# Kernel optimization log

Hardware: AMD Instinct MI355X
Metric: run time of the kernel (lower is better)

Reference implementation:

```python
import jax, jax.numpy as jnp
import numpy as np

STATE_DIM = 256
LATENT_DIM = 64
HIDDEN = 64
NUM_EMB = 2048
BATCH = 32768


def setup_inputs() -> dict:
    key = jax.random.key(0)
    ks = jax.random.split(key, 10)
    s = lambda *sh: 1.0 / np.sqrt(sh[0])
    return {
        "x": jax.random.normal(ks[0], (BATCH, STATE_DIM), dtype=jnp.float32),
        # encoder: Linear(state_dim, 64) -> ReLU -> Linear(64, latent_dim)
        "enc_w1": jax.random.uniform(ks[1], (STATE_DIM, HIDDEN), jnp.float32, -s(STATE_DIM), s(STATE_DIM)),
        "enc_b1": jax.random.uniform(ks[2], (HIDDEN,), jnp.float32, -s(STATE_DIM), s(STATE_DIM)),
        "enc_w2": jax.random.uniform(ks[3], (HIDDEN, LATENT_DIM), jnp.float32, -s(HIDDEN), s(HIDDEN)),
        "enc_b2": jax.random.uniform(ks[4], (LATENT_DIM,), jnp.float32, -s(HIDDEN), s(HIDDEN)),
        # codebook
        "emb": jax.random.normal(ks[5], (NUM_EMB, LATENT_DIM), dtype=jnp.float32),
        # decoder: Linear(latent_dim, 64) -> ReLU -> Linear(64, state_dim)
        "dec_w1": jax.random.uniform(ks[6], (LATENT_DIM, HIDDEN), jnp.float32, -s(LATENT_DIM), s(LATENT_DIM)),
        "dec_b1": jax.random.uniform(ks[7], (HIDDEN,), jnp.float32, -s(LATENT_DIM), s(LATENT_DIM)),
        "dec_w2": jax.random.uniform(ks[8], (HIDDEN, STATE_DIM), jnp.float32, -s(HIDDEN), s(HIDDEN)),
        "dec_b2": jax.random.uniform(ks[9], (STATE_DIM,), jnp.float32, -s(HIDDEN), s(HIDDEN)),
    }


def reference(x, enc_w1, enc_b1, enc_w2, enc_b2, emb, dec_w1, dec_b1, dec_w2, dec_b2):
    # encoder MLP: z_e [B, latent]
    h = jax.nn.relu(x @ enc_w1 + enc_b1)
    z_e = h @ enc_w2 + enc_b2
    # squared euclidean distances to codebook, expanded form: [B, K]
    # ||z - e||^2 = ||z||^2 - 2 z.e + ||e||^2  (same argmin as broadcast form)
    d = (jnp.sum(z_e * z_e, axis=1, keepdims=True)
         - 2.0 * (z_e @ emb.T)
         + jnp.sum(emb * emb, axis=1)[None, :])
    z_q_idx = jnp.argmin(d, axis=1)           # [B]
    z_q = emb[z_q_idx]                        # [B, latent]
    # decoder MLP
    hd = jax.nn.relu(z_q @ dec_w1 + dec_b1)
    x_recon = hd @ dec_w2 + dec_b2
    return (x_recon, z_e, z_q)
```

## Files before the change

### kernel.cpp

```cpp
#include <hip/hip_runtime.h>

#define BATCH   32768
#define SD      256
#define LD      64
#define HDIM    64
#define NEMB    2048
#define REFINE_THR_Q 5e-4f

typedef short  short8 __attribute__((ext_vector_type(8)));
typedef float  f32x4  __attribute__((ext_vector_type(4)));

__device__ __forceinline__ unsigned short f2bf(float f) {
    unsigned int u = __float_as_uint(f);
    u = (u + 0x7FFFu + ((u >> 16) & 1u)) >> 16;
    return (unsigned short)u;
}
__device__ __forceinline__ float bf2f(unsigned short h) {
    return __uint_as_float(((unsigned int)h) << 16);
}

__global__ __launch_bounds__(256) void k0_all(const float* __restrict__ emb,
                                              const float* __restrict__ dw1,
                                              const float* __restrict__ dw2,
                                              const float* __restrict__ ew1,
                                              const float* __restrict__ ew2,
                                              float* __restrict__ e2q,
                                              unsigned short* __restrict__ eh,
                                              unsigned short* __restrict__ el,
                                              unsigned short* __restrict__ w1h,
                                              unsigned short* __restrict__ w1l,
                                              unsigned short* __restrict__ w2h,
                                              unsigned short* __restrict__ w2l,
                                              unsigned short* __restrict__ w1eh,
                                              unsigned short* __restrict__ w1em,
                                              unsigned short* __restrict__ w1el,
                                              unsigned short* __restrict__ w2eh,
                                              unsigned short* __restrict__ w2em,
                                              unsigned short* __restrict__ w2el,
                                              int* __restrict__ count) {
    int b = blockIdx.x;
    int t = threadIdx.x;
    if (b < 8) {
        int k = b * 256 + t;
        if (k == 0) *count = 0;
        const float* er = emb + (size_t)k * LD;
        unsigned short hrow[LD], lrow[LD];
        float s = 0.f;
#pragma unroll
        for (int q = 0; q < LD; ++q) {
            float v = er[q];
            s += v * v;
            unsigned short h = f2bf(v);
            hrow[q] = h;
            lrow[q] = f2bf(v - bf2f(h));
        }
        e2q[k] = -0.5f * s;
        short8* dh = (short8*)(eh + (size_t)k * LD);
        short8* dl = (short8*)(el + (size_t)k * LD);
#pragma unroll
        for (int q = 0; q < 8; ++q) {
            dh[q] = *(short8*)&hrow[q * 8];
            dl[q] = *(short8*)&lrow[q * 8];
        }
    } else if (b < 24) {
        int e = (b - 8) * 256 + t;
        int j = e >> 6, k = e & 63;
        float v = dw1[k * HDIM + j];
        unsigned short h = f2bf(v);
        w1h[e] = h; w1l[e] = f2bf(v - bf2f(h));
    } else if (b < 88) {
        int e = (b - 24) * 256 + t;
        int j = e >> 6, k = e & 63;
        float v = dw2[k * SD + j];
        unsigned short h = f2bf(v);
        w2h[e] = h; w2l[e] = f2bf(v - bf2f(h));
    } else if (b < 152) {
        int e = (b - 88) * 256 + t;
        int kt = e >> 11, j = (e & 2047) >> 5, kk = e & 31;
        int k = kt * 32 + kk;
        float v = ew1[k * HDIM + j];
        unsigned short h = f2bf(v);
        float r1 = v - bf2f(h);
        unsigned short m = f2bf(r1);
        float r2 = r1 - bf2f(m);
        w1eh[e] = h; w1em[e] = m; w1el[e] = f2bf(r2);
    } else {
        int e = (b - 152) * 256 + t;
        int kt = e >> 11, j = (e & 2047) >> 5, kk = e & 31;
        int k = kt * 32 + kk;
        float v = ew2[k * LD + j];
        unsigned short h = f2bf(v);
        float r1 = v - bf2f(h);
        unsigned short m = f2bf(r1);
        float r2 = r1 - bf2f(m);
        w2eh[e] = h; w2em[e] = m; w2el[e] = f2bf(r2);
    }
}

#define MF(Afr, Bfr, C) __builtin_amdgcn_mfma_f32_16x16x32_bf16(Afr, Bfr, C, 0, 0, 0)

#define E_WLOAD(P, KT, JT) do {                                             \
    size_t wo_ = (size_t)(KT) * 2048 + ((JT) * 16 + lo) * 32 + hi * 8;      \
    P##h = *(const short8*)(w1eh + wo_);                                    \
    P##m = *(const short8*)(w1em + wo_);                                    \
    P##l = *(const short8*)(w1el + wo_);                                    \
} while (0)

#define E_COMP(P, JT) do {                                                  \
    f32x4 c_ = c1[JT];                                                      \
    c_ = MF(xl8, P##h, c_);                                                 \
    c_ = MF(xm8, P##m, c_);                                                 \
    c_ = MF(xh8, P##l, c_);                                                 \
    c_ = MF(xm8, P##h, c_);                                                 \
    c_ = MF(xh8, P##m, c_);                                                 \
    c_ = MF(xh8, P##h, c_);                                                 \
    c1[JT] = c_;                                                            \
} while (0)

__global__ __launch_bounds__(256, 2) void k_enc(const float* __restrict__ x,
                                                const unsigned short* __restrict__ w1eh,
                                                const unsigned short* __restrict__ w1em,
                                                const unsigned short* __restrict__ w1el,
                                                const float* __restrict__ b1,
                                                const unsigned short* __restrict__ w2eh,
                                                const unsigned short* __restrict__ w2em,
                                                const unsigned short* __restrict__ w2el,
                                                const float* __restrict__ b2,
                                                float* __restrict__ zOut,
                                                unsigned short* __restrict__ zh,
                                                unsigned short* __restrict__ zl) {
    __shared__ float hds[4][16 * 68];
    int tid  = threadIdx.x;
    int lane = tid & 63;
    int w    = tid >> 6;
    int lo   = lane & 15;
    int hi   = lane >> 4;
    int rb   = blockIdx.x * 64 + w * 16;
    int row  = rb + lo;
    const float* xrow = x + (size_t)row * SD;

    f32x4 c1[4];
#pragma unroll
    for (int jt = 0; jt < 4; ++jt) {
        float bj = b1[jt * 16 + lo];
        f32x4 c = {bj, bj, bj, bj};
        c1[jt] = c;
    }

    short8 Ph, Pm, Pl, Qh, Qm, Ql, Rh, Rm, Rl, Sh, Sm, Sl;
    float4 xc0, xc1, xn0, xn1;
    xc0 = *(const float4*)(xrow + hi * 8);
    xc1 = *(const float4*)(xrow + hi * 8 + 4);
    E_WLOAD(P, 0, 0); E_WLOAD(Q, 0, 1); E_WLOAD(R, 0, 2); E_WLOAD(S, 0, 3);

#pragma unroll 1
    for (int kt = 0; kt < 8; ++kt) {
        int ktn = (kt + 1) & 7;
        xn0 = *(const float4*)(xrow + ktn * 32 + hi * 8);
        xn1 = *(const float4*)(xrow + ktn * 32 + hi * 8 + 4);

        float v[8] = {xc0.x, xc0.y, xc0.z, xc0.w, xc1.x, xc1.y, xc1.z, xc1.w};
        unsigned short sh[8], sm[8], sl[8];
#pragma unroll
        for (int q = 0; q < 8; ++q) {
            unsigned short h = f2bf(v[q]);
            float r1 = v[q] - bf2f(h);
            unsigned short m = f2bf(r1);
            float r2 = r1 - bf2f(m);
            sh[q] = h; sm[q] = m; sl[q] = f2bf(r2);
        }
        short8 xh8 = *(short8*)sh, xm8 = *(short8*)sm, xl8 = *(short8*)sl;

        E_COMP(P, 0); E_WLOAD(P, ktn, 0);
        E_COMP(Q, 1); E_WLOAD(Q, ktn, 1);
        E_COMP(R, 2); E_WLOAD(R, ktn, 2);
        E_COMP(S, 3); E_WLOAD(S, ktn, 3);
        xc0 = xn0; xc1 = xn1;
    }

#pragma unroll
    for (int jt = 0; jt < 4; ++jt)
#pragma unroll
        for (int r = 0; r < 4; ++r)
            hds[w][(hi * 4 + r) * 68 + jt * 16 + lo] = fmaxf(c1[jt][r], 0.f);
    __syncthreads();

    f32x4 c2[4];
#pragma unroll
    for (int jt = 0; jt < 4; ++jt) {
        float bj = b2[jt * 16 + lo];
        f32x4 c = {bj, bj, bj, bj};
        c2[jt] = c;
    }
#pragma unroll
    for (int kt = 0; kt < 2; ++kt) {
        float4 a4 = *(const float4*)&hds[w][lo * 68 + kt * 32 + hi * 8];
        float4 b4 = *(const float4*)&hds[w][lo * 68 + kt * 32 + hi * 8 + 4];
        float v[8] = {a4.x, a4.y, a4.z, a4.w, b4.x, b4.y, b4.z, b4.w};
        unsigned short sh[8], sm[8], sl[8];
#pragma unroll
        for (int q = 0; q < 8; ++q) {
            unsigned short h = f2bf(v[q]);
            float r1 = v[q] - bf2f(h);
            unsigned short m = f2bf(r1);
            float r2 = r1 - bf2f(m);
            sh[q] = h; sm[q] = m; sl[q] = f2bf(r2);
        }
        short8 ah = *(short8*)sh, am = *(short8*)sm, al = *(short8*)sl;
#pragma unroll
        for (int jt = 0; jt < 4; ++jt) {
            size_t wo = (size_t)kt * 2048 + (jt * 16 + lo) * 32 + hi * 8;
            short8 bh8 = *(const short8*)(w2eh + wo);
            short8 bm8 = *(const short8*)(w2em + wo);
            short8 bl8 = *(const short8*)(w2el + wo);
            f32x4 c = c2[jt];
            c = MF(al, bh8, c);
            c = MF(am, bm8, c);
            c = MF(ah, bl8, c);
            c = MF(am, bh8, c);
            c = MF(ah, bm8, c);
            c = MF(ah, bh8, c);
            c2[jt] = c;
        }
    }
#pragma unroll
    for (int jt = 0; jt < 4; ++jt) {
#pragma unroll
        for (int r = 0; r < 4; ++r) {
            float z = c2[jt][r];
            size_t o = (size_t)(rb + hi * 4 + r) * LD + jt * 16 + lo;
            zOut[o] = z;
            unsigned short hb = f2bf(z);
            zh[o] = hb;
            zl[o] = f2bf(z - bf2f(hb));
        }
    }
}

#define K2_LOAD(P, t) do {                                                  \
    const unsigned short* ph_ = ehp + (size_t)(t) * 16 * LD;                \
    const unsigned short* pl_ = elp + (size_t)(t) * 16 * LD;                \
    P##a0 = *(const short8*)(ph_);                                          \
    P##a1 = *(const short8*)(ph_ + 32);                                     \
    P##a2 = *(const short8*)(pl_);                                          \
    P##a3 = *(const short8*)(pl_ + 32);                                     \
    P##e2 = *(const f32x4*)(e2q + cbase + (t) * 16 + hi * 4);               \
} while (0)

#define K2_COMP(P, t) do {                                                  \
    f32x4 acc_[4];                                                          \
    _Pragma("unroll")                                                       \
    for (int g = 0; g < 4; ++g) {                                           \
        f32x4 c_;                                                           \
        c_ = __builtin_amdgcn_mfma_f32_16x16x32_bf16(P##a0, bh[g][0], P##e2, 0, 0, 0); \
        c_ = __builtin_amdgcn_mfma_f32_16x16x32_bf16(P##a1, bh[g][1], c_, 0, 0, 0);    \
        c_ = __builtin_amdgcn_mfma_f32_16x16x32_bf16(P##a2, bh[g][0], c_, 0, 0, 0);    \
        c_ = __builtin_amdgcn_mfma_f32_16x16x32_bf16(P##a3, bh[g][1], c_, 0, 0, 0);    \
        c_ = __builtin_amdgcn_mfma_f32_16x16x32_bf16(P##a0, bl[g][0], c_, 0, 0, 0);    \
        c_ = __builtin_amdgcn_mfma_f32_16x16x32_bf16(P##a1, bl[g][1], c_, 0, 0, 0);    \
        acc_[g] = c_;                                                       \
    }                                                                       \
    _Pragma("unroll")                                                       \
    for (int g = 0; g < 4; ++g) {                                           \
        float m_ = fmaxf(fmaxf(acc_[g][0], acc_[g][1]),                     \
                         fmaxf(acc_[g][2], acc_[g][3]));                    \
        bool win_ = (m_ > bb[g]);                                           \
        qv[g] = win_ ? acc_[g] : qv[g];                                     \
        tt[g] = win_ ? (t) : tt[g];                                         \
        b2v[g] = fmaxf(b2v[g], fminf(bb[g], m_));                           \
        bb[g] = fmaxf(bb[g], m_);                                           \
    }                                                                       \
} while (0)

__global__ __launch_bounds__(256, 2) void k2_mfma(const unsigned short* __restrict__ zh,
                                                  const unsigned short* __restrict__ zl,
                                                  const unsigned short* __restrict__ eh,
                                                  const unsigned short* __restrict__ el,
                                                  const float* __restrict__ e2q,
                                                  int* __restrict__ idx,
                                                  int* __restrict__ list,
                                                  int* __restrict__ count) {
    int tid  = threadIdx.x;
    int lane = tid & 63;
    int w    = tid >> 6;
    int rb   = blockIdx.x * 64;
    int lo   = lane & 15;
    int hi   = lane >> 4;

    short8 bh[4][2], bl[4][2];
#pragma unroll
    for (int g = 0; g < 4; ++g) {
        size_t zo = (size_t)(rb + g * 16 + lo) * LD + hi * 8;
        bh[g][0] = *(const short8*)(zh + zo);
        bh[g][1] = *(const short8*)(zh + zo + 32);
        bl[g][0] = *(const short8*)(zl + zo);
        bl[g][1] = *(const short8*)(zl + zo + 32);
    }

    float bb[4], b2v[4];
    f32x4 qv[4];
    int   tt[4];
#pragma unroll
    for (int g = 0; g < 4; ++g) {
        bb[g] = -3.0e38f; b2v[g] = -3.0e38f; tt[g] = 0;
        qv[g][0] = qv[g][1] = qv[g][2] = qv[g][3] = -3.0e38f;
    }

    const int cbase = w * (NEMB / 4);
    const unsigned short* ehp = eh + (size_t)(cbase + lo) * LD + hi * 8;
    const unsigned short* elp = el + (size_t)(cbase + lo) * LD + hi * 8;

    short8 Aa0, Aa1, Aa2, Aa3; f32x4 Ae2;
    short8 Ba0, Ba1, Ba2, Ba3; f32x4 Be2;
    short8 Ca0, Ca1, Ca2, Ca3; f32x4 Ce2;

    K2_LOAD(A, 0);
    K2_LOAD(B, 1);
    K2_LOAD(C, 2);

    for (int tb = 0; tb < 27; tb += 3) {
        K2_COMP(A, tb);     K2_LOAD(A, tb + 3);
        K2_COMP(B, tb + 1); K2_LOAD(B, tb + 4);
        K2_COMP(C, tb + 2); K2_LOAD(C, tb + 5);
    }
    K2_COMP(A, 27); K2_LOAD(A, 30);
    K2_COMP(B, 28); K2_LOAD(B, 31);
    K2_COMP(C, 29);
    K2_COMP(A, 30);
    K2_COMP(B, 31);

    float ss[4];
    int   ii[4];
#pragma unroll
    for (int g = 0; g < 4; ++g) {
        float s0 = qv[g][0], s1 = qv[g][1], s2 = qv[g][2], s3 = qv[g][3];
        float M01 = fmaxf(s0, s1), L01 = fminf(s0, s1);
        float M23 = fmaxf(s2, s3), L23 = fminf(s2, s3);
        int   d01 = (s1 > s0) ? 1 : 0;
        int   d23 = (s3 > s2) ? 3 : 2;
        bool  cp  = (M23 > M01);
        float within2 = fmaxf(fminf(M01, M23), cp ? L23 : L01);
        int   dd  = cp ? d23 : d01;
        ii[g] = cbase + tt[g] * 16 + hi * 4 + dd;
        ss[g] = fmaxf(b2v[g], within2);
    }

#pragma unroll
    for (int off = 16; off <= 32; off <<= 1) {
#pragma unroll
        for (int g = 0; g < 4; ++g) {
            float ob = __shfl_xor(bb[g], off);
            float os = __shfl_xor(ss[g], off);
            int   oi = __shfl_xor(ii[g], off);
            ss[g] = fmaxf(fmaxf(fminf(bb[g], ob), os), ss[g]);
            ii[g] = (ob > bb[g]) ? oi : ii[g];
            bb[g] = fmaxf(bb[g], ob);
        }
    }

    __shared__ float Lb[4][64];
    __shared__ float Ls[4][64];
    __shared__ int   Li[4][64];
    if (lane < 16) {
#pragma unroll
        for (int g = 0; g < 4; ++g) {
            Lb[w][g * 16 + lane] = bb[g];
            Ls[w][g * 16 + lane] = ss[g];
            Li[w][g * 16 + lane] = ii[g];
        }
    }
    __syncthreads();

    if (tid < 64) {
        float B = Lb[0][tid], S = Ls[0][tid];
        int   I = Li[0][tid];
#pragma unroll
        for (int w2 = 1; w2 < 4; ++w2) {
            float ob = Lb[w2][tid], os = Ls[w2][tid];
            int   oi = Li[w2][tid];
            S = fmaxf(fmaxf(fminf(B, ob), os), S);
            I = (ob > B) ? oi : I;
            B = fmaxf(B, ob);
        }
        idx[rb + tid] = I;
        if (B - S < REFINE_THR_Q) {
            int p = atomicAdd(count, 1);
            list[p] = rb + tid;
        }
    }
}

__global__ __launch_bounds__(256) void k3_refine(const float* __restrict__ z,
                                                 const float* __restrict__ emb,
                                                 const int* __restrict__ count,
                                                 const int* __restrict__ list,
                                                 int* __restrict__ idx) {
    __shared__ double sv[256];
    __shared__ int    sx[256];
    int tid = threadIdx.x;
    int n = *count;
    for (int g = blockIdx.x; g < n; g += gridDim.x) {
        int row = list[g];
        const float4* zr4 = (const float4*)(z + (size_t)row * LD);
        float4 zv[16];
#pragma unroll
        for (int q = 0; q < 16; ++q) zv[q] = zr4[q];

        double best = 1.0e300;
        int bi = NEMB;
#pragma unroll 2
        for (int c = 0; c < 8; ++c) {
            int k = tid * 8 + c;
            const float4* er = (const float4*)(emb + (size_t)k * LD);
            double d0 = 0.0, d1 = 0.0, d2 = 0.0, d3 = 0.0;
#pragma unroll
            for (int q = 0; q < 16; ++q) {
                float4 e4 = er[q];
                double tx = (double)zv[q].x - (double)e4.x;
                double ty = (double)zv[q].y - (double)e4.y;
                double tz = (double)zv[q].z - (double)e4.z;
                double tw = (double)zv[q].w - (double)e4.w;
                d0 += tx * tx; d1 += ty * ty; d2 += tz * tz; d3 += tw * tw;
            }
            double d = (d0 + d1) + (d2 + d3);
            if (d < best) { best = d; bi = k; }
        }
        sv[tid] = best; sx[tid] = bi;
        __syncthreads();
        for (int s = 128; s > 0; s >>= 1) {
            if (tid < s) {
                if (sv[tid + s] < sv[tid] ||
                    (sv[tid + s] == sv[tid] && sx[tid + s] < sx[tid])) {
                    sv[tid] = sv[tid + s]; sx[tid] = sx[tid + s];
                }
            }
            __syncthreads();
        }
        if (tid == 0) idx[row] = sx[0];
        __syncthreads();
    }
}

__global__ __launch_bounds__(256, 2) void k_dec(const int* __restrict__ idx,
                                                const float* __restrict__ emb,
                                                const unsigned short* __restrict__ w1h,
                                                const unsigned short* __restrict__ w1l,
                                                const float* __restrict__ b1,
                                                const unsigned short* __restrict__ w2h,
                                                const unsigned short* __restrict__ w2l,
                                                const float* __restrict__ b2,
                                                float* __restrict__ xrec,
                                                float* __restrict__ zq) {
    __shared__ float hds[4][16 * 68];
    int tid  = threadIdx.x;
    int lane = tid & 63;
    int w    = tid >> 6;
    int lo   = lane & 15;
    int hi   = lane >> 4;
    int rb   = blockIdx.x * 64 + w * 16;
    int row  = rb + lo;
    int ix   = idx[row];

    short8 zah[2], zal[2];
    {
        const float* er  = emb + (size_t)ix * LD + hi * 8;
        float* zqr = zq + (size_t)row * LD + hi * 8;
#pragma unroll
        for (int kt = 0; kt < 2; ++kt) {
            float4 a = *(const float4*)(er + kt * 32);
            float4 b = *(const float4*)(er + kt * 32 + 4);
            *(float4*)(zqr + kt * 32) = a;
            *(float4*)(zqr + kt * 32 + 4) = b;
            float v[8] = {a.x, a.y, a.z, a.w, b.x, b.y, b.z, b.w};
            unsigned short hh[8], ll[8];
#pragma unroll
            for (int q = 0; q < 8; ++q) {
                unsigned short hb = f2bf(v[q]);
                hh[q] = hb;
                ll[q] = f2bf(v[q] - bf2f(hb));
            }
            zah[kt] = *(short8*)hh;
            zal[kt] = *(short8*)ll;
        }
    }

#pragma unroll
    for (int jt = 0; jt < 4; ++jt) {
        float bj = b1[jt * 16 + lo];
        f32x4 c = {bj, bj, bj, bj};
#pragma unroll
        for (int kt = 0; kt < 2; ++kt) {
            short8 bh8 = *(const short8*)(w1h + (jt * 16 + lo) * LD + kt * 32 + hi * 8);
            short8 bl8 = *(const short8*)(w1l + (jt * 16 + lo) * LD + kt * 32 + hi * 8);
            c = __builtin_amdgcn_mfma_f32_16x16x32_bf16(zah[kt], bh8, c, 0, 0, 0);
            c = __builtin_amdgcn_mfma_f32_16x16x32_bf16(zah[kt], bl8, c, 0, 0, 0);
            c = __builtin_amdgcn_mfma_f32_16x16x32_bf16(zal[kt], bh8, c, 0, 0, 0);
        }
#pragma unroll
        for (int r = 0; r < 4; ++r)
            hds[w][(hi * 4 + r) * 68 + jt * 16 + lo] = fmaxf(c[r], 0.f);
    }
    __syncthreads();

    short8 hah[2], hal[2];
#pragma unroll
    for (int kt = 0; kt < 2; ++kt) {
        float4 a = *(const float4*)&hds[w][lo * 68 + kt * 32 + hi * 8];
        float4 b = *(const float4*)&hds[w][lo * 68 + kt * 32 + hi * 8 + 4];
        float v[8] = {a.x, a.y, a.z, a.w, b.x, b.y, b.z, b.w};
        unsigned short hh[8], ll[8];
#pragma unroll
        for (int q = 0; q < 8; ++q) {
            unsigned short hb = f2bf(v[q]);
            hh[q] = hb;
            ll[q] = f2bf(v[q] - bf2f(hb));
        }
        hah[kt] = *(short8*)hh;
        hal[kt] = *(short8*)ll;
    }

    for (int jt = 0; jt < 16; ++jt) {
        float bj = b2[jt * 16 + lo];
        f32x4 c = {bj, bj, bj, bj};
#pragma unroll
        for (int kt = 0; kt < 2; ++kt) {
            short8 bh8 = *(const short8*)(w2h + (jt * 16 + lo) * LD + kt * 32 + hi * 8);
            short8 bl8 = *(const short8*)(w2l + (jt * 16 + lo) * LD + kt * 32 + hi * 8);
            c = __builtin_amdgcn_mfma_f32_16x16x32_bf16(hah[kt], bh8, c, 0, 0, 0);
            c = __builtin_amdgcn_mfma_f32_16x16x32_bf16(hah[kt], bl8, c, 0, 0, 0);
            c = __builtin_amdgcn_mfma_f32_16x16x32_bf16(hal[kt], bh8, c, 0, 0, 0);
        }
#pragma unroll
        for (int r = 0; r < 4; ++r)
            xrec[(size_t)(rb + hi * 4 + r) * SD + jt * 16 + lo] = c[r];
    }
}

extern "C" void kernel_launch(void* const* d_in, const int* in_sizes, int n_in,
                              void* d_out, int out_size, void* d_ws, size_t ws_size,
                              hipStream_t stream) {
    const float* x   = (const float*)d_in[0];
    const float* ew1 = (const float*)d_in[1];
    const float* eb1 = (const float*)d_in[2];
    const float* ew2 = (const float*)d_in[3];
    const float* eb2 = (const float*)d_in[4];
    const float* emb = (const float*)d_in[5];
    const float* dw1 = (const float*)d_in[6];
    const float* db1 = (const float*)d_in[7];
    const float* dw2 = (const float*)d_in[8];
    const float* db2 = (const float*)d_in[9];

    float* out  = (float*)d_out;
    float* xrec = out;
    float* zE   = out + (size_t)BATCH * SD;
    float* zQ   = zE + (size_t)BATCH * LD;

    char* xb = (char*)xrec;
    unsigned short* zh   = (unsigned short*)xb;
    unsigned short* zl   = (unsigned short*)(xb + (4u << 20));
    unsigned short* eh   = (unsigned short*)(xb + (8u << 20));
    unsigned short* el   = (unsigned short*)(xb + (8u << 20) + (NEMB * LD * 2));
    float*          e2q  = (float*)(xb + (9u << 20));
    unsigned short* w1eh = (unsigned short*)(xb + (10u << 20));
    unsigned short* w1em = w1eh + 16384;
    unsigned short* w1el = w1em + 16384;
    unsigned short* w2eh = w1el + 16384;
    unsigned short* w2em = w2eh + 4096;
    unsigned short* w2el = w2em + 4096;

    char* ws = (char*)d_ws;
    int*  count = (int*)ws;
    int*  idxA  = (int*)(ws + 16384);
    int*  list  = (int*)(ws + 147456);
    unsigned short* w1h = (unsigned short*)(ws + 278528);
    unsigned short* w1l = (unsigned short*)(ws + 286720);
    unsigned short* w2h = (unsigned short*)(ws + 294912);
    unsigned short* w2l = (unsigned short*)(ws + 327680);

    hipLaunchKernelGGL(k0_all,    dim3(168),        dim3(256), 0, stream,
                       emb, dw1, dw2, ew1, ew2, e2q, eh, el,
                       w1h, w1l, w2h, w2l, w1eh, w1em, w1el, w2eh, w2em, w2el, count);
    hipLaunchKernelGGL(k_enc,     dim3(BATCH / 64), dim3(256), 0, stream,
                       x, w1eh, w1em, w1el, eb1, w2eh, w2em, w2el, eb2, zE, zh, zl);
    hipLaunchKernelGGL(k2_mfma,   dim3(BATCH / 64), dim3(256), 0, stream,
                       zh, zl, eh, el, e2q, idxA, list, count);
    hipLaunchKernelGGL(k3_refine, dim3(128),        dim3(256), 0, stream,
                       zE, emb, count, list, idxA);
    hipLaunchKernelGGL(k_dec,     dim3(BATCH / 64), dim3(256), 0, stream,
                       idxA, emb, w1h, w1l, db1, w2h, w2l, db2, xrec, zQ);
}
```

Before: 117.3 us.

## Fuse encoder MLP into codebook distance kernel via shared-memory z handoff

Merges the encoder kernel and the MFMA distance/argmin kernel into a single launch. The bf16 hi/lo split of z_e now goes into reused shared memory instead of global scratch buffers, removing a launch and the global write and read of zh/zl. The cost is higher register and LDS pressure in the fused kernel, which could lower occupancy at the same launch bounds.

```diff
diff --git a/kernel.cpp b/kernel.cpp
--- a/kernel.cpp
+++ b/kernel.cpp
@@ -117,126 +117,6 @@
     c1[JT] = c_;                                                            \
 } while (0)
 
-__global__ __launch_bounds__(256, 2) void k_enc(const float* __restrict__ x,
-                                                const unsigned short* __restrict__ w1eh,
-                                                const unsigned short* __restrict__ w1em,
-                                                const unsigned short* __restrict__ w1el,
-                                                const float* __restrict__ b1,
-                                                const unsigned short* __restrict__ w2eh,
-                                                const unsigned short* __restrict__ w2em,
-                                                const unsigned short* __restrict__ w2el,
-                                                const float* __restrict__ b2,
-                                                float* __restrict__ zOut,
-                                                unsigned short* __restrict__ zh,
-                                                unsigned short* __restrict__ zl) {
-    __shared__ float hds[4][16 * 68];
-    int tid  = threadIdx.x;
-    int lane = tid & 63;
-    int w    = tid >> 6;
-    int lo   = lane & 15;
-    int hi   = lane >> 4;
-    int rb   = blockIdx.x * 64 + w * 16;
-    int row  = rb + lo;
-    const float* xrow = x + (size_t)row * SD;
-
-    f32x4 c1[4];
-#pragma unroll
-    for (int jt = 0; jt < 4; ++jt) {
-        float bj = b1[jt * 16 + lo];
-        f32x4 c = {bj, bj, bj, bj};
-        c1[jt] = c;
-    }
-
-    short8 Ph, Pm, Pl, Qh, Qm, Ql, Rh, Rm, Rl, Sh, Sm, Sl;
-    float4 xc0, xc1, xn0, xn1;
-    xc0 = *(const float4*)(xrow + hi * 8);
-    xc1 = *(const float4*)(xrow + hi * 8 + 4);
-    E_WLOAD(P, 0, 0); E_WLOAD(Q, 0, 1); E_WLOAD(R, 0, 2); E_WLOAD(S, 0, 3);
-
-#pragma unroll 1
-    for (int kt = 0; kt < 8; ++kt) {
-        int ktn = (kt + 1) & 7;
-        xn0 = *(const float4*)(xrow + ktn * 32 + hi * 8);
-        xn1 = *(const float4*)(xrow + ktn * 32 + hi * 8 + 4);
-
-        float v[8] = {xc0.x, xc0.y, xc0.z, xc0.w, xc1.x, xc1.y, xc1.z, xc1.w};
-        unsigned short sh[8], sm[8], sl[8];
-#pragma unroll
-        for (int q = 0; q < 8; ++q) {
-            unsigned short h = f2bf(v[q]);
-            float r1 = v[q] - bf2f(h);
-            unsigned short m = f2bf(r1);
-            float r2 = r1 - bf2f(m);
-            sh[q] = h; sm[q] = m; sl[q] = f2bf(r2);
-        }
-        short8 xh8 = *(short8*)sh, xm8 = *(short8*)sm, xl8 = *(short8*)sl;
-
-        E_COMP(P, 0); E_WLOAD(P, ktn, 0);
-        E_COMP(Q, 1); E_WLOAD(Q, ktn, 1);
-        E_COMP(R, 2); E_WLOAD(R, ktn, 2);
-        E_COMP(S, 3); E_WLOAD(S, ktn, 3);
-        xc0 = xn0; xc1 = xn1;
-    }
-
-#pragma unroll
-    for (int jt = 0; jt < 4; ++jt)
-#pragma unroll
-        for (int r = 0; r < 4; ++r)
-            hds[w][(hi * 4 + r) * 68 + jt * 16 + lo] = fmaxf(c1[jt][r], 0.f);
-    __syncthreads();
-
-    f32x4 c2[4];
-#pragma unroll
-    for (int jt = 0; jt < 4; ++jt) {
-        float bj = b2[jt * 16 + lo];
-        f32x4 c = {bj, bj, bj, bj};
-        c2[jt] = c;
-    }
-#pragma unroll
-    for (int kt = 0; kt < 2; ++kt) {
-        float4 a4 = *(const float4*)&hds[w][lo * 68 + kt * 32 + hi * 8];
-        float4 b4 = *(const float4*)&hds[w][lo * 68 + kt * 32 + hi * 8 + 4];
-        float v[8] = {a4.x, a4.y, a4.z, a4.w, b4.x, b4.y, b4.z, b4.w};
-        unsigned short sh[8], sm[8], sl[8];
-#pragma unroll
-        for (int q = 0; q < 8; ++q) {
-            unsigned short h = f2bf(v[q]);
-            float r1 = v[q] - bf2f(h);
-            unsigned short m = f2bf(r1);
-            float r2 = r1 - bf2f(m);
-            sh[q] = h; sm[q] = m; sl[q] = f2bf(r2);
-        }
-        short8 ah = *(short8*)sh, am = *(short8*)sm, al = *(short8*)sl;
-#pragma unroll
-        for (int jt = 0; jt < 4; ++jt) {
-            size_t wo = (size_t)kt * 2048 + (jt * 16 + lo) * 32 + hi * 8;
-            short8 bh8 = *(const short8*)(w2eh + wo);
-            short8 bm8 = *(const short8*)(w2em + wo);
-            short8 bl8 = *(const short8*)(w2el + wo);
-            f32x4 c = c2[jt];
-            c = MF(al, bh8, c);
-            c = MF(am, bm8, c);
-            c = MF(ah, bl8, c);
-            c = MF(am, bh8, c);
-            c = MF(ah, bm8, c);
-            c = MF(ah, bh8, c);
-            c2[jt] = c;
-        }
-    }
-#pragma unroll
-    for (int jt = 0; jt < 4; ++jt) {
-#pragma unroll
-        for (int r = 0; r < 4; ++r) {
-            float z = c2[jt][r];
-            size_t o = (size_t)(rb + hi * 4 + r) * LD + jt * 16 + lo;
-            zOut[o] = z;
-            unsigned short hb = f2bf(z);
-            zh[o] = hb;
-            zl[o] = f2bf(z - bf2f(hb));
-        }
-    }
-}
-
 #define K2_LOAD(P, t) do {                                                  \
     const unsigned short* ph_ = ehp + (size_t)(t) * 16 * LD;                \
     const unsigned short* pl_ = elp + (size_t)(t) * 16 * LD;                \
@@ -272,29 +152,148 @@
     }                                                                       \
 } while (0)
 
-__global__ __launch_bounds__(256, 2) void k2_mfma(const unsigned short* __restrict__ zh,
-                                                  const unsigned short* __restrict__ zl,
+__global__ __launch_bounds__(256, 2) void k_fused(const float* __restrict__ x,
+                                                  const unsigned short* __restrict__ w1eh,
+                                                  const unsigned short* __restrict__ w1em,
+                                                  const unsigned short* __restrict__ w1el,
+                                                  const float* __restrict__ b1,
+                                                  const unsigned short* __restrict__ w2eh,
+                                                  const unsigned short* __restrict__ w2em,
+                                                  const unsigned short* __restrict__ w2el,
+                                                  const float* __restrict__ b2,
                                                   const unsigned short* __restrict__ eh,
                                                   const unsigned short* __restrict__ el,
                                                   const float* __restrict__ e2q,
+                                                  float* __restrict__ zOut,
                                                   int* __restrict__ idx,
                                                   int* __restrict__ list,
                                                   int* __restrict__ count) {
+    __shared__ float hds[4][16 * 68];
+    unsigned short* zlsH = (unsigned short*)hds;
+    unsigned short* zlsL = (unsigned short*)hds + 64 * 68;
+    __shared__ float Lb[4][64];
+    __shared__ float Ls[4][64];
+    __shared__ int   Li[4][64];
+
     int tid  = threadIdx.x;
     int lane = tid & 63;
     int w    = tid >> 6;
-    int rb   = blockIdx.x * 64;
     int lo   = lane & 15;
     int hi   = lane >> 4;
+    int rb   = blockIdx.x * 64;
+    int rbw  = rb + w * 16;
+    int row  = rbw + lo;
+    const float* xrow = x + (size_t)row * SD;
+
+    f32x4 c1[4];
+#pragma unroll
+    for (int jt = 0; jt < 4; ++jt) {
+        float bj = b1[jt * 16 + lo];
+        f32x4 c = {bj, bj, bj, bj};
+        c1[jt] = c;
+    }
+
+    short8 Ph, Pm, Pl, Qh, Qm, Ql, Rh, Rm, Rl, Sh, Sm, Sl;
+    float4 xc0, xc1, xn0, xn1;
+    xc0 = *(const float4*)(xrow + hi * 8);
+    xc1 = *(const float4*)(xrow + hi * 8 + 4);
+    E_WLOAD(P, 0, 0); E_WLOAD(Q, 0, 1); E_WLOAD(R, 0, 2); E_WLOAD(S, 0, 3);
+
+#pragma unroll 1
+    for (int kt = 0; kt < 8; ++kt) {
+        int ktn = (kt + 1) & 7;
+        xn0 = *(const float4*)(xrow + ktn * 32 + hi * 8);
+        xn1 = *(const float4*)(xrow + ktn * 32 + hi * 8 + 4);
+
+        float v[8] = {xc0.x, xc0.y, xc0.z, xc0.w, xc1.x, xc1.y, xc1.z, xc1.w};
+        unsigned short sh[8], sm[8], sl[8];
+#pragma unroll
+        for (int q = 0; q < 8; ++q) {
+            unsigned short h = f2bf(v[q]);
+            float r1 = v[q] - bf2f(h);
+            unsigned short m = f2bf(r1);
+            float r2 = r1 - bf2f(m);
+            sh[q] = h; sm[q] = m; sl[q] = f2bf(r2);
+        }
+        short8 xh8 = *(short8*)sh, xm8 = *(short8*)sm, xl8 = *(short8*)sl;
+
+        E_COMP(P, 0); E_WLOAD(P, ktn, 0);
+        E_COMP(Q, 1); E_WLOAD(Q, ktn, 1);
+        E_COMP(R, 2); E_WLOAD(R, ktn, 2);
+        E_COMP(S, 3); E_WLOAD(S, ktn, 3);
+        xc0 = xn0; xc1 = xn1;
+    }
+
+#pragma unroll
+    for (int jt = 0; jt < 4; ++jt)
+#pragma unroll
+        for (int r = 0; r < 4; ++r)
+            hds[w][(hi * 4 + r) * 68 + jt * 16 + lo] = fmaxf(c1[jt][r], 0.f);
+    __syncthreads();
+
+    f32x4 c2[4];
+#pragma unroll
+    for (int jt = 0; jt < 4; ++jt) {
+        float bj = b2[jt * 16 + lo];
+        f32x4 c = {bj, bj, bj, bj};
+        c2[jt] = c;
+    }
+#pragma unroll
+    for (int kt = 0; kt < 2; ++kt) {
+        float4 a4 = *(const float4*)&hds[w][lo * 68 + kt * 32 + hi * 8];
+        float4 b4 = *(const float4*)&hds[w][lo * 68 + kt * 32 + hi * 8 + 4];
+        float v[8] = {a4.x, a4.y, a4.z, a4.w, b4.x, b4.y, b4.z, b4.w};
+        unsigned short sh[8], sm[8], sl[8];
+#pragma unroll
+        for (int q = 0; q < 8; ++q) {
+            unsigned short h = f2bf(v[q]);
+            float r1 = v[q] - bf2f(h);
+            unsigned short m = f2bf(r1);
+            float r2 = r1 - bf2f(m);
+            sh[q] = h; sm[q] = m; sl[q] = f2bf(r2);
+        }
+        short8 ah = *(short8*)sh, am = *(short8*)sm, al = *(short8*)sl;
+#pragma unroll
+        for (int jt = 0; jt < 4; ++jt) {
+            size_t wo = (size_t)kt * 2048 + (jt * 16 + lo) * 32 + hi * 8;
+            short8 bh8 = *(const short8*)(w2eh + wo);
+            short8 bm8 = *(const short8*)(w2em + wo);
+            short8 bl8 = *(const short8*)(w2el + wo);
+            f32x4 c = c2[jt];
+            c = MF(al, bh8, c);
+            c = MF(am, bm8, c);
+            c = MF(ah, bl8, c);
+            c = MF(am, bh8, c);
+            c = MF(ah, bm8, c);
+            c = MF(ah, bh8, c);
+            c2[jt] = c;
+        }
+    }
+    __syncthreads();
+
+#pragma unroll
+    for (int jt = 0; jt < 4; ++jt) {
+#pragma unroll
+        for (int r = 0; r < 4; ++r) {
+            float z = c2[jt][r];
+            int lrow = w * 16 + hi * 4 + r;
+            int col  = jt * 16 + lo;
+            zOut[(size_t)(rb + lrow) * LD + col] = z;
+            unsigned short hb = f2bf(z);
+            zlsH[lrow * 68 + col] = hb;
+            zlsL[lrow * 68 + col] = f2bf(z - bf2f(hb));
+        }
+    }
+    __syncthreads();
 
     short8 bh[4][2], bl[4][2];
 #pragma unroll
     for (int g = 0; g < 4; ++g) {
-        size_t zo = (size_t)(rb + g * 16 + lo) * LD + hi * 8;
-        bh[g][0] = *(const short8*)(zh + zo);
-        bh[g][1] = *(const short8*)(zh + zo + 32);
-        bl[g][0] = *(const short8*)(zl + zo);
-        bl[g][1] = *(const short8*)(zl + zo + 32);
+        int lr = g * 16 + lo;
+        bh[g][0] = *(const short8*)&zlsH[lr * 68 + hi * 8];
+        bh[g][1] = *(const short8*)&zlsH[lr * 68 + 32 + hi * 8];
+        bl[g][0] = *(const short8*)&zlsL[lr * 68 + hi * 8];
+        bl[g][1] = *(const short8*)&zlsL[lr * 68 + 32 + hi * 8];
     }
 
     float bb[4], b2v[4];
@@ -358,9 +357,6 @@
         }
     }
 
-    __shared__ float Lb[4][64];
-    __shared__ float Ls[4][64];
-    __shared__ int   Li[4][64];
     if (lane < 16) {
 #pragma unroll
         for (int g = 0; g < 4; ++g) {
@@ -556,8 +552,6 @@
     float* zQ   = zE + (size_t)BATCH * LD;
 
     char* xb = (char*)xrec;
-    unsigned short* zh   = (unsigned short*)xb;
-    unsigned short* zl   = (unsigned short*)(xb + (4u << 20));
     unsigned short* eh   = (unsigned short*)(xb + (8u << 20));
     unsigned short* el   = (unsigned short*)(xb + (8u << 20) + (NEMB * LD * 2));
     float*          e2q  = (float*)(xb + (9u << 20));
@@ -580,10 +574,9 @@
     hipLaunchKernelGGL(k0_all,    dim3(168),        dim3(256), 0, stream,
                        emb, dw1, dw2, ew1, ew2, e2q, eh, el,
                        w1h, w1l, w2h, w2l, w1eh, w1em, w1el, w2eh, w2em, w2el, count);
-    hipLaunchKernelGGL(k_enc,     dim3(BATCH / 64), dim3(256), 0, stream,
-                       x, w1eh, w1em, w1el, eb1, w2eh, w2em, w2el, eb2, zE, zh, zl);
-    hipLaunchKernelGGL(k2_mfma,   dim3(BATCH / 64), dim3(256), 0, stream,
-                       zh, zl, eh, el, e2q, idxA, list, count);
+    hipLaunchKernelGGL(k_fused,   dim3(BATCH / 64), dim3(256), 0, stream,
+                       x, w1eh, w1em, w1el, eb1, w2eh, w2em, w2el, eb2,
+                       eh, el, e2q, zE, idxA, list, count);
     hipLaunchKernelGGL(k3_refine, dim3(128),        dim3(256), 0, stream,
                        zE, emb, count, list, idxA);
     hipLaunchKernelGGL(k_dec,     dim3(BATCH / 64), dim3(256), 0, stream,
```

Measured after the change: 111.1 us, median of 2. -5.3%, faster.
